# Optimization experiments

Measured on AMD Instinct MI355X. Metric: run time of the kernel, lower is better.

## Reference

```python
import jax, jax.numpy as jnp
import numpy as np

BETA = 0.9
PI = 3.141592653589793

# snntorch Leaky with ATan surrogate (alpha=2): fwd = heaviside, bwd = 1/(1+(pi*x)^2)
@jax.custom_vjp
def spike_fn(x):
    return (x > 0).astype(x.dtype)

def _spike_fwd(x):
    return spike_fn(x), x

def _spike_bwd(x, g):
    return (g / (1.0 + (PI * x) ** 2),)

spike_fn.defvjp(_spike_fwd, _spike_bwd)

def lif_step(mem, cur, thr):
    # snntorch Leaky (reset_mechanism='subtract'):
    #   reset computed from OLD mem (detached), spike from NEW mem
    reset = jax.lax.stop_gradient((mem - thr > 0).astype(mem.dtype))
    mem_new = BETA * mem + cur - reset * thr
    spk = spike_fn(mem_new - thr)
    return spk, mem_new

def setup_inputs() -> dict:
    key = jax.random.key(0)
    ks = jax.random.split(key, 2)
    B, C, T = 8192, 1, 4096
    spike_input = jax.random.normal(ks[0], (B, C, T), dtype=jnp.float32)
    f32 = lambda v: jnp.array([v], dtype=jnp.float32)
    return {
        'spike_input': spike_input,
        'w_n1': f32(0.5), 'w_n2': f32(0.4),
        'w_n3_1': f32(0.6), 'w_n3_2': f32(0.6),
        'w_inh': f32(0.3), 'w_inh_n3': f32(-0.5),
        'thr_n1': f32(0.5), 'thr_n2': f32(0.5),
        'thr_n3': f32(0.5), 'thr_inh': f32(0.5),
    }

def reference(spike_input, w_n1, w_n2, w_n3_1, w_n3_2, w_inh, w_inh_n3,
              thr_n1, thr_n2, thr_n3, thr_inh):
    # (B, C, T) -> (B, T): mean over channels (== squeeze when C==1)
    x = spike_input.mean(axis=1) if spike_input.ndim == 3 else spike_input
    xt = x.T  # (T, B) for scan over time

    def step(carry, x_t):
        m1, m2, m3, mi = carry
        s1, m1 = lif_step(m1, x_t * w_n1[0], thr_n1[0])
        s2, m2 = lif_step(m2, x_t * w_n2[0], thr_n2[0])
        si, mi = lif_step(mi, x_t * w_inh[0], thr_inh[0])
        cur3 = s1 * w_n3_1[0] + s2 * w_n3_2[0] + si * w_inh_n3[0]
        s3, m3 = lif_step(m3, cur3, thr_n3[0])
        return (m1, m2, m3, mi), (s1, s2, s3, si)

    init = tuple(jnp.zeros_like(xt[0]) for _ in range(4))
    _, (s1, s2, s3, si) = jax.lax.scan(step, init, xt)
    trigger = s3.mean(axis=0)[:, None]  # (B, 1)
    return trigger, s1.T, s2.T, s3.T, si.T
```

## Files before the change

### kernel.cpp

```cpp
#include <hip/hip_runtime.h>
#include <stdint.h>


constexpr int Bn = 8192;
constexpr int Tn = 4096;
constexpr int SEG = 512;
constexpr int NSEG = Tn / SEG;
constexpr int WUP = 384;

typedef float v4f __attribute__((ext_vector_type(4)));

struct SnnState { float m1, m2, m3, mi, s1, s2, s3, si; };

__device__ __forceinline__ void lif_step(SnnState& S, float xx,
    float w1, float w2, float w31, float w32, float wi, float wi3,
    float th1, float th2, float th3, float thi)
{
    const float BETA = 0.9f;
    float c1 = xx * w1;
    S.m1 = __builtin_fmaf(BETA, S.m1, c1);
    S.m1 = __builtin_fmaf(-S.s1, th1, S.m1);
    S.s1 = (S.m1 > th1) ? 1.0f : 0.0f;
    float c2 = xx * w2;
    S.m2 = __builtin_fmaf(BETA, S.m2, c2);
    S.m2 = __builtin_fmaf(-S.s2, th2, S.m2);
    S.s2 = (S.m2 > th2) ? 1.0f : 0.0f;
    float ci = xx * wi;
    S.mi = __builtin_fmaf(BETA, S.mi, ci);
    S.mi = __builtin_fmaf(-S.si, thi, S.mi);
    S.si = (S.mi > thi) ? 1.0f : 0.0f;
    float cur3 = S.s1 * w31;
    cur3 = __builtin_fmaf(S.s2, w32, cur3);
    cur3 = __builtin_fmaf(S.si, wi3, cur3);
    S.m3 = __builtin_fmaf(BETA, S.m3, cur3);
    S.m3 = __builtin_fmaf(-S.s3, th3, S.m3);
    S.s3 = (S.m3 > th3) ? 1.0f : 0.0f;
}


__global__ __launch_bounds__(64) void snn_fused_kernel(
    const float* __restrict__ x, float* __restrict__ out,
    uint32_t* __restrict__ counts,
    const float* __restrict__ pw1,  const float* __restrict__ pw2,
    const float* __restrict__ pw31, const float* __restrict__ pw32,
    const float* __restrict__ pwi,  const float* __restrict__ pwi3,
    const float* __restrict__ pt1,  const float* __restrict__ pt2,
    const float* __restrict__ pt3,  const float* __restrict__ pti)
{
    __shared__ uint32_t lbits[2][64][4];
    const int lane = threadIdx.x;
    const int seg  = blockIdx.y;
    const int r0   = blockIdx.x * 64;
    const int b    = r0 + lane;
    const int t0   = seg * SEG;
    const int ts   = (t0 - WUP > 0) ? (t0 - WUP) : 0;
    const int nwu  = (t0 - ts) / 32;
    const int nc   = nwu + SEG / 32;

    const float w1  = pw1[0],  w2  = pw2[0];
    const float w31 = pw31[0], w32 = pw32[0];
    const float wi  = pwi[0],  wi3 = pwi3[0];
    const float th1 = pt1[0],  th2 = pt2[0];
    const float th3 = pt3[0],  thi = pti[0];

    const float4* xw = reinterpret_cast<const float4*>(x + (size_t)b * Tn + ts);

    const int lrow = lane >> 3;
    const int lq   = lane & 7;
    float* obase = out + Bn + (size_t)(r0 + lrow) * Tn + t0 + lq * 4;
    const size_t BT = (size_t)Bn * Tn;

    SnnState S = {0.f,0.f,0.f,0.f, 0.f,0.f,0.f,0.f};
    uint32_t cnt = 0;

    auto process = [&](const float4 (&buf)[8], int c) {
        if (c < nwu) {
            #pragma unroll
            for (int v = 0; v < 8; ++v) {
                const float xsv[4] = {buf[v].x, buf[v].y, buf[v].z, buf[v].w};
                #pragma unroll
                for (int k = 0; k < 4; ++k)
                    lif_step(S, xsv[k], w1,w2,w31,w32,wi,wi3,th1,th2,th3,thi);
            }
        } else {
            float bl1=0.f,bl2=0.f,bl3=0.f,bl4=0.f, bh1=0.f,bh2=0.f,bh3=0.f,bh4=0.f;
            #pragma unroll
            for (int v = 0; v < 8; ++v) {
                const float xsv[4] = {buf[v].x, buf[v].y, buf[v].z, buf[v].w};
                #pragma unroll
                for (int k = 0; k < 4; ++k) {
                    lif_step(S, xsv[k], w1,w2,w31,w32,wi,wi3,th1,th2,th3,thi);
                    const int kk = v * 4 + k;
                    const float pw = (float)(1u << (kk & 15));
                    if (kk < 16) {
                        bl1 = __builtin_fmaf(S.s1, pw, bl1);
                        bl2 = __builtin_fmaf(S.s2, pw, bl2);
                        bl3 = __builtin_fmaf(S.s3, pw, bl3);
                        bl4 = __builtin_fmaf(S.si, pw, bl4);
                    } else {
                        bh1 = __builtin_fmaf(S.s1, pw, bh1);
                        bh2 = __builtin_fmaf(S.s2, pw, bh2);
                        bh3 = __builtin_fmaf(S.s3, pw, bh3);
                        bh4 = __builtin_fmaf(S.si, pw, bh4);
                    }
                }
            }
            const int ce = c - nwu;
            const int pb = ce & 1;
            const uint32_t u0 = (uint32_t)bl1 | ((uint32_t)bh1 << 16);
            const uint32_t u1 = (uint32_t)bl2 | ((uint32_t)bh2 << 16);
            const uint32_t u2 = (uint32_t)bl3 | ((uint32_t)bh3 << 16);
            const uint32_t u3 = (uint32_t)bl4 | ((uint32_t)bh4 << 16);
            lbits[pb][lane][0] = u0;
            lbits[pb][lane][1] = u1;
            lbits[pb][lane][2] = u2;
            lbits[pb][lane][3] = u3;
            cnt += __popc(u2);
            asm volatile("s_waitcnt lgkmcnt(0)" ::: "memory");
            float* oc = obase + ce * 32;
            #pragma unroll
            for (int s = 0; s < 4; ++s) {
                #pragma unroll
                for (int rg = 0; rg < 8; ++rg) {
                    const uint32_t w  = lbits[pb][rg * 8 + lrow][s];
                    const uint32_t sh = w >> (lq * 4);
                    v4f f;
                    f.x = (float)( sh       & 1u);
                    f.y = (float)((sh >> 1) & 1u);
                    f.z = (float)((sh >> 2) & 1u);
                    f.w = (float)((sh >> 3) & 1u);
                    __builtin_nontemporal_store(
                        f, reinterpret_cast<v4f*>(
                               oc + (size_t)s * BT + (size_t)rg * 8 * Tn));
                }
            }
        }
    };

    float4 bufA[8], bufB[8];
    #pragma unroll
    for (int i = 0; i < 8; ++i) bufA[i] = xw[i];

    for (int c = 0; c < nc; c += 2) {
        #pragma unroll
        for (int i = 0; i < 8; ++i) bufB[i] = xw[(c + 1) * 8 + i];
        process(bufA, c);
        if (c + 2 < nc) {
            #pragma unroll
            for (int i = 0; i < 8; ++i) bufA[i] = xw[(c + 2) * 8 + i];
        }
        process(bufB, c + 1);
    }
    counts[(size_t)seg * Bn + b] = cnt;
}


__global__ __launch_bounds__(256) void snn_trigger_kernel(
    const uint32_t* __restrict__ counts, float* __restrict__ out)
{
    const int b = blockIdx.x * 256 + threadIdx.x;
    uint32_t t = 0;
    #pragma unroll
    for (int s = 0; s < NSEG; ++s) t += counts[(size_t)s * Bn + b];
    out[b] = (float)t * (1.0f / 4096.0f);
}


constexpr int CH = 32;
constexpr int NV = CH / 4;

__device__ __forceinline__ void run_chunk_f(
    const float4 (&xb)[NV], SnnState& S, float& accf,
    float* __restrict__ o1, float* __restrict__ o2,
    float* __restrict__ o3, float* __restrict__ o4, int t0,
    float w1, float w2, float w31, float w32, float wi, float wi3,
    float th1, float th2, float th3, float thi)
{
    #pragma unroll
    for (int v = 0; v < NV; ++v) {
        const float xsv[4] = {xb[v].x, xb[v].y, xb[v].z, xb[v].w};
        float r1[4], r2[4], r3[4], r4[4];
        #pragma unroll
        for (int k = 0; k < 4; ++k) {
            lif_step(S, xsv[k], w1,w2,w31,w32,wi,wi3,th1,th2,th3,thi);
            accf += S.s3;
            r1[k] = S.s1; r2[k] = S.s2; r3[k] = S.s3; r4[k] = S.si;
        }
        *reinterpret_cast<float4*>(o1 + t0 + v * 4) = make_float4(r1[0], r1[1], r1[2], r1[3]);
        *reinterpret_cast<float4*>(o2 + t0 + v * 4) = make_float4(r2[0], r2[1], r2[2], r2[3]);
        *reinterpret_cast<float4*>(o3 + t0 + v * 4) = make_float4(r3[0], r3[1], r3[2], r3[3]);
        *reinterpret_cast<float4*>(o4 + t0 + v * 4) = make_float4(r4[0], r4[1], r4[2], r4[3]);
    }
}

__global__ __launch_bounds__(64) void snn_scan_kernel(
    const float* __restrict__ x, float* __restrict__ out,
    const float* __restrict__ pw1,  const float* __restrict__ pw2,
    const float* __restrict__ pw31, const float* __restrict__ pw32,
    const float* __restrict__ pwi,  const float* __restrict__ pwi3,
    const float* __restrict__ pt1,  const float* __restrict__ pt2,
    const float* __restrict__ pt3,  const float* __restrict__ pti)
{
    const int b = blockIdx.x * 64 + threadIdx.x;
    const float w1  = pw1[0],  w2  = pw2[0];
    const float w31 = pw31[0], w32 = pw32[0];
    const float wi  = pwi[0],  wi3 = pwi3[0];
    const float th1 = pt1[0],  th2 = pt2[0];
    const float th3 = pt3[0],  thi = pti[0];

    const float4* xr = reinterpret_cast<const float4*>(x + (size_t)b * Tn);
    float* o1 = out + Bn + (size_t)b * Tn;
    float* o2 = o1 + (size_t)Bn * Tn;
    float* o3 = o2 + (size_t)Bn * Tn;
    float* o4 = o3 + (size_t)Bn * Tn;

    float4 bufA[NV], bufB[NV];
    #pragma unroll
    for (int i = 0; i < NV; ++i) bufA[i] = xr[i];
    SnnState S = {0.f,0.f,0.f,0.f, 0.f,0.f,0.f,0.f};
    float accf = 0.f;

    for (int t0 = 0; t0 < Tn; t0 += 2 * CH) {
        const int tB = t0 + CH;
        const int tA = t0 + 2 * CH;
        #pragma unroll
        for (int i = 0; i < NV; ++i) bufB[i] = xr[tB / 4 + i];
        run_chunk_f(bufA, S, accf, o1, o2, o3, o4, t0,
                    w1, w2, w31, w32, wi, wi3, th1, th2, th3, thi);
        if (tA < Tn) {
            #pragma unroll
            for (int i = 0; i < NV; ++i) bufA[i] = xr[tA / 4 + i];
        }
        run_chunk_f(bufB, S, accf, o1, o2, o3, o4, tB,
                    w1, w2, w31, w32, wi, wi3, th1, th2, th3, thi);
    }
    out[b] = accf * (1.0f / 4096.0f);
}

extern "C" void kernel_launch(void* const* d_in, const int* in_sizes, int n_in,
                              void* d_out, int out_size, void* d_ws, size_t ws_size,
                              hipStream_t stream) {
    const float* x = (const float*)d_in[0];
    float* out = (float*)d_out;
    const size_t counts_bytes = (size_t)NSEG * Bn * 4;

    if (d_ws != nullptr && ws_size >= counts_bytes) {
        uint32_t* counts = (uint32_t*)d_ws;
        snn_fused_kernel<<<dim3(Bn / 64, NSEG), dim3(64), 0, stream>>>(
            x, out, counts,
            (const float*)d_in[1], (const float*)d_in[2],
            (const float*)d_in[3], (const float*)d_in[4],
            (const float*)d_in[5], (const float*)d_in[6],
            (const float*)d_in[7], (const float*)d_in[8],
            (const float*)d_in[9], (const float*)d_in[10]);
        snn_trigger_kernel<<<dim3(Bn / 256), dim3(256), 0, stream>>>(counts, out);
    } else {
        snn_scan_kernel<<<dim3(Bn / 64), dim3(64), 0, stream>>>(
            x, out,
            (const float*)d_in[1], (const float*)d_in[2],
            (const float*)d_in[3], (const float*)d_in[4],
            (const float*)d_in[5], (const float*)d_in[6],
            (const float*)d_in[7], (const float*)d_in[8],
            (const float*)d_in[9], (const float*)d_in[10]);
    }
}
```

Before: 138.9 us.

## Batch spike-bit writeback over 8 chunks for full-row coalesced stores

```diff
diff --git a/kernel.cpp b/kernel.cpp
--- a/kernel.cpp
+++ b/kernel.cpp
@@ -47,7 +47,7 @@
     const float* __restrict__ pt1,  const float* __restrict__ pt2,
     const float* __restrict__ pt3,  const float* __restrict__ pti)
 {
-    __shared__ uint32_t lbits[2][64][4];
+    __shared__ uint32_t lb[2][4][64][9];
     const int lane = threadIdx.x;
     const int seg  = blockIdx.y;
     const int r0   = blockIdx.x * 64;
@@ -65,9 +65,8 @@
 
     const float4* xw = reinterpret_cast<const float4*>(x + (size_t)b * Tn + ts);
 
-    const int lrow = lane >> 3;
-    const int lq   = lane & 7;
-    float* obase = out + Bn + (size_t)(r0 + lrow) * Tn + t0 + lq * 4;
+    const int lw  = lane >> 3;
+    const int lsh = (lane & 7) * 4;
     const size_t BT = (size_t)Bn * Tn;
 
     SnnState S = {0.f,0.f,0.f,0.f, 0.f,0.f,0.f,0.f};
@@ -105,33 +104,35 @@
                     }
                 }
             }
-            const int ce = c - nwu;
-            const int pb = ce & 1;
-            const uint32_t u0 = (uint32_t)bl1 | ((uint32_t)bh1 << 16);
-            const uint32_t u1 = (uint32_t)bl2 | ((uint32_t)bh2 << 16);
+            const int ce  = c - nwu;
+            const int rnd = ce >> 3;
+            const int pb  = rnd & 1;
+            const int w   = ce & 7;
             const uint32_t u2 = (uint32_t)bl3 | ((uint32_t)bh3 << 16);
-            const uint32_t u3 = (uint32_t)bl4 | ((uint32_t)bh4 << 16);
-            lbits[pb][lane][0] = u0;
-            lbits[pb][lane][1] = u1;
-            lbits[pb][lane][2] = u2;
-            lbits[pb][lane][3] = u3;
+            lb[pb][0][lane][w] = (uint32_t)bl1 | ((uint32_t)bh1 << 16);
+            lb[pb][1][lane][w] = (uint32_t)bl2 | ((uint32_t)bh2 << 16);
+            lb[pb][2][lane][w] = u2;
+            lb[pb][3][lane][w] = (uint32_t)bl4 | ((uint32_t)bh4 << 16);
             cnt += __popc(u2);
-            asm volatile("s_waitcnt lgkmcnt(0)" ::: "memory");
-            float* oc = obase + ce * 32;
-            #pragma unroll
-            for (int s = 0; s < 4; ++s) {
-                #pragma unroll
-                for (int rg = 0; rg < 8; ++rg) {
-                    const uint32_t w  = lbits[pb][rg * 8 + lrow][s];
-                    const uint32_t sh = w >> (lq * 4);
-                    v4f f;
-                    f.x = (float)( sh       & 1u);
-                    f.y = (float)((sh >> 1) & 1u);
-                    f.z = (float)((sh >> 2) & 1u);
-                    f.w = (float)((sh >> 3) & 1u);
-                    __builtin_nontemporal_store(
-                        f, reinterpret_cast<v4f*>(
-                               oc + (size_t)s * BT + (size_t)rg * 8 * Tn));
+            if (w == 7) {
+                asm volatile("s_waitcnt lgkmcnt(0)" ::: "memory");
+                float* op = out + Bn + (size_t)r0 * Tn
+                          + (t0 + rnd * 256) + 4 * lane;
+                #pragma unroll 1
+                for (int s = 0; s < 4; ++s) {
+                    float* ops = op + (size_t)s * BT;
+                    #pragma unroll 8
+                    for (int row = 0; row < 64; ++row) {
+                        const uint32_t wv = lb[pb][s][row][lw];
+                        const uint32_t sh = wv >> lsh;
+                        v4f f;
+                        f.x = (float)( sh       & 1u);
+                        f.y = (float)((sh >> 1) & 1u);
+                        f.z = (float)((sh >> 2) & 1u);
+                        f.w = (float)((sh >> 3) & 1u);
+                        __builtin_nontemporal_store(
+                            f, reinterpret_cast<v4f*>(ops + (size_t)row * Tn));
+                    }
                 }
             }
         }
```

After: 138.1 us. About the same (-0.5%).
